# Optimization experiments

Hardware: AMD Instinct MI355X
Metric: run time of the kernel (lower is better)

The kernel has to match this reference:

```python
import jax, jax.numpy as jnp
import numpy as np

B, O, D = 4096, 256, 256  # batch, size_out (rules), size_in (features)


def setup_inputs() -> dict:
    key = jax.random.key(0)
    k1, k2, k3, k4, k5 = jax.random.split(key, 5)
    return {
        "x": jax.random.normal(k1, (B, D), dtype=jnp.float32),
        "scales": jax.random.normal(k2, (O, D), dtype=jnp.float32),
        # strict upper triangle holds the packed rot vectors (original inits them to zeros;
        # small values keep the quadratic form well conditioned)
        "rots": jax.random.normal(k3, (O, D, D), dtype=jnp.float32) * 0.02,
        "centroids": jax.random.normal(k4, (O, D, 1), dtype=jnp.float32),
        "b": jax.random.uniform(k5, (O,), dtype=jnp.float32, minval=0.5, maxval=1.5),
    }


def reference(x, scales, rots, centroids, b):
    # Build symmetric transform A[o] = diag(scales[o]) + triu(rots[o],1) + triu(rots[o],1)^T
    # (equivalent to the loop of diag_embed(r_i, i+1) + mirrored lower diagonal).
    upper = jnp.triu(rots, 1)                                   # [O,D,D]
    A = upper + jnp.swapaxes(upper, -1, -2)
    A = A + jnp.eye(D, dtype=scales.dtype) * scales[:, None, :]  # diag_embed(scales)
    # Augmented affine map: mul[o,i,b'] = A[o] @ x[b'] + centroid[o,i]; const row dropped
    # since only the first size_in rows feed the norm.
    y = jnp.einsum('bj,oij->boi', x, A) + centroids[..., 0][None, :, :]  # [B,O,D]
    rx = jnp.sqrt(jnp.sum(y * y, axis=-1))                      # L2 norm over D -> [B,O]
    return 1.0 / (1.0 + rx ** (2.0 * b))                        # bell membership [B,O]
```

## Files before the change

kernel.cpp:

```cpp
#include <hip/hip_runtime.h>
#include <cstdint>
#include <cmath>

#define Bn 4096
#define Dn 256
#define On 256

typedef __bf16 v8bf __attribute__((ext_vector_type(8)));
typedef float  v16f __attribute__((ext_vector_type(16)));
typedef unsigned short us8 __attribute__((ext_vector_type(8)));

__device__ __forceinline__ unsigned short f2bf(float f) {
    unsigned int u = __builtin_bit_cast(unsigned int, f);
    unsigned int r = (u + 0x7fffu + ((u >> 16) & 1u)) >> 16;
    return (unsigned short)r;
}

__device__ __forceinline__ void gl_lds16(const void* g, void* l) {
    __builtin_amdgcn_global_load_lds(
        (const __attribute__((address_space(1))) void*)(uintptr_t)g,
        (__attribute__((address_space(3))) void*)(uintptr_t)l, 16, 0, 0);
}

__global__ __launch_bounds__(256) void prep_x(const float* __restrict__ x,
                                              unsigned short* __restrict__ xbT) {
    __shared__ float t[64][68];
    const int tid = threadIdx.x;
    const int bb = blockIdx.x >> 2;
    const int kb = blockIdx.x & 3;
    const int b0 = bb * 64;
#pragma unroll
    for (int s = 0; s < 4; ++s) {
        const int idx = s * 256 + tid;
        const int r = idx >> 4, c4 = idx & 15;
        const float4 v = *(const float4*)(x + (size_t)(b0 + r) * Dn + kb * 64 + c4 * 4);
        *(float4*)&t[r][c4 * 4] = v;
    }
    __syncthreads();
    const int lane = tid & 63, wv = tid >> 6;
#pragma unroll
    for (int s = 0; s < 2; ++s) {
        const int kcl = s * 4 + wv;
        us8 u;
#pragma unroll
        for (int q = 0; q < 8; ++q) u[q] = f2bf(t[lane][kcl * 8 + q]);
        *(us8*)(xbT + ((size_t)(kb * 8 + kcl) * Bn + b0 + lane) * 8) = u;
    }
}

template <int TI, int TJ>
__device__ __forceinline__ void extract_pair(const float* T, v8bf (&af)[16],
                                             float sc, int wv, int lane) {
    const int l31 = lane & 31, hw = lane >> 5;
    const int half = wv & 1, grp = wv >> 1;
    if (TI == TJ) {
        if (grp == TI) {
            const int r = half * 32 + l31;
            const int mr = (r & 7) << 2;
#pragma unroll
            for (int kq = 0; kq < 4; ++kq) {
                us8 u;
#pragma unroll
                for (int q = 0; q < 8; ++q) {
                    const int c = kq * 16 + hw * 8 + q;
                    const float v = (r < c) ? T[r * 64 + (c ^ mr)]
                                  : ((r > c) ? T[c * 64 + (r ^ ((c & 7) << 2))]
                                             : sc);
                    u[q] = f2bf(v);
                }
                af[TI * 4 + kq] = __builtin_bit_cast(v8bf, u);
            }
        }
    } else {
        if (grp == TI) {
            const int r = half * 32 + l31;
            const int mr = (r & 7) << 2;
#pragma unroll
            for (int kq = 0; kq < 4; ++kq) {
                const int c0 = kq * 16 + hw * 8;
                const float4 a = *(const float4*)&T[r * 64 + (c0 ^ mr)];
                const float4 b = *(const float4*)&T[r * 64 + ((c0 + 4) ^ mr)];
                us8 u;
                u[0] = f2bf(a.x); u[1] = f2bf(a.y); u[2] = f2bf(a.z); u[3] = f2bf(a.w);
                u[4] = f2bf(b.x); u[5] = f2bf(b.y); u[6] = f2bf(b.z); u[7] = f2bf(b.w);
                af[TJ * 4 + kq] = __builtin_bit_cast(v8bf, u);
            }
        } else if (grp == TJ) {
            const int cL = half * 32 + l31;
#pragma unroll
            for (int kq = 0; kq < 4; ++kq) {
                us8 u;
#pragma unroll
                for (int q = 0; q < 8; ++q) {
                    const int rL = kq * 16 + hw * 8 + q;
                    u[q] = f2bf(T[rL * 64 + (cL ^ ((rL & 7) << 2))]);
                }
                af[TI * 4 + kq] = __builtin_bit_cast(v8bf, u);
            }
        }
    }
}

#define WAITV(N)                                              \
    do {                                                      \
        asm volatile("s_waitcnt vmcnt(" #N ")" ::: "memory"); \
        __builtin_amdgcn_sched_barrier(0);                    \
    } while (0)
#define LGKM0()                                               \
    do {                                                      \
        asm volatile("s_waitcnt lgkmcnt(0)" ::: "memory");    \
        __builtin_amdgcn_sched_barrier(0);                    \
    } while (0)
#define BARF()                                                \
    do {                                                      \
        __builtin_amdgcn_sched_barrier(0);                    \
        __builtin_amdgcn_s_barrier();                         \
        __builtin_amdgcn_sched_barrier(0);                    \
    } while (0)

#define STAGE_T(TIv, TJv, DST)                                               \
    do {                                                                     \
        const float* s_ = rbase + (TIv) * (64 * Dn) + (TJv) * 64;            \
        _Pragma("unroll")                                                    \
        for (int s = 0; s < 2; ++s) {                                        \
            const int idx = s * 512 + tid;                                   \
            const int r = idx >> 4, c4 = idx & 15;                           \
            gl_lds16(s_ + (size_t)r * Dn + ((c4 ^ (r & 7)) * 4),             \
                     (DST) + idx * 4);                                       \
        }                                                                    \
    } while (0)

__global__ __launch_bounds__(512, 4) void fuzzy_main(
    const float* __restrict__ rots, const float* __restrict__ scales,
    const unsigned short* __restrict__ xbT, const float* __restrict__ cent,
    const float* __restrict__ bvals, float* __restrict__ out) {
    __shared__ __align__(16) unsigned short Xs[2][2048][8];
    __shared__ float ssbuf[2][8][64];
    __shared__ float centL[Dn];

    const int tid  = threadIdx.x;
    const int lane = tid & 63;
    const int wv   = tid >> 6;
    const int l31  = lane & 31, hw = lane >> 5;
    const int Lb = blockIdx.x;
    const int o     = (Lb & 7) * 32 + ((Lb >> 3) & 31);
    const int bhalf = Lb >> 8;
    const int bh0   = bhalf * 2048;

    if (tid < Dn) centL[tid] = cent[o * Dn + tid];
    const float sc = scales[o * Dn + wv * 32 + l31];
    const float bv = bvals[o];

    WAITV(0);

    float* const S0 = (float*)&Xs[0][0][0];
    float* const S1 = S0 + 4096;
    float* const S2 = (float*)&Xs[1][0][0];
    float* const S3 = S2 + 4096;
    const float* const rbase = rots + ((size_t)o << 16);

    v8bf af[16];

    STAGE_T(0, 1, S0); STAGE_T(2, 3, S1);
    STAGE_T(0, 2, S2); STAGE_T(1, 3, S3);
    WAITV(4); BARF();
    extract_pair<0, 1>(S0, af, sc, wv, lane);
    extract_pair<2, 3>(S1, af, sc, wv, lane);
    LGKM0(); BARF();
    STAGE_T(0, 3, S0); STAGE_T(1, 2, S1);
    WAITV(4); BARF();
    extract_pair<0, 2>(S2, af, sc, wv, lane);
    extract_pair<1, 3>(S3, af, sc, wv, lane);
    LGKM0(); BARF();
    STAGE_T(0, 0, S2); STAGE_T(1, 1, S3);
    WAITV(4); BARF();
    extract_pair<0, 3>(S0, af, sc, wv, lane);
    extract_pair<1, 2>(S1, af, sc, wv, lane);
    LGKM0(); BARF();
    STAGE_T(2, 2, S0); STAGE_T(3, 3, S1);
    WAITV(4); BARF();
    extract_pair<0, 0>(S2, af, sc, wv, lane);
    extract_pair<1, 1>(S3, af, sc, wv, lane);
    LGKM0(); BARF();
    WAITV(0); BARF();
    extract_pair<2, 2>(S0, af, sc, wv, lane);
    extract_pair<3, 3>(S1, af, sc, wv, lane);
    LGKM0(); BARF();

    const unsigned short* px[4];
#pragma unroll
    for (int s = 0; s < 4; ++s)
        px[s] = xbT + ((size_t)(s * 8 + wv) * Bn + bh0 + lane) * 8;

#pragma unroll
    for (int s = 0; s < 4; ++s)
        gl_lds16(px[s], &Xs[0][s * 512 + tid][0]);
    __syncthreads();

    for (int it = 0; it < 32; ++it) {
        const int buf = it & 1;
        if (it < 31) {
#pragma unroll
            for (int s = 0; s < 4; ++s) {
                px[s] += 512;
                gl_lds16(px[s], &Xs[buf ^ 1][s * 512 + tid][0]);
            }
        }

        if (it >= 1 && lane < 8) {
            const int bl = wv * 8 + lane;
            float ssq = 0.f;
#pragma unroll
            for (int w = 0; w < 8; ++w) ssq += ssbuf[buf ^ 1][w][bl];
            out[(size_t)(bh0 + (it - 1) * 64 + bl) * On + o] =
                1.0f / (1.0f + exp2f(bv * log2f(ssq)));
        }

        v16f acc[2];
#pragma unroll
        for (int nt = 0; nt < 2; ++nt)
#pragma unroll
            for (int rg = 0; rg < 16; ++rg) acc[nt][rg] = 0.f;

#pragma unroll
        for (int ks = 0; ks < 16; ++ks) {
            const v8bf xf0 = *(const v8bf*)&Xs[buf][(ks * 2 + hw) * 64 + l31][0];
            const v8bf xf1 = *(const v8bf*)&Xs[buf][(ks * 2 + hw) * 64 + 32 + l31][0];
            acc[0] = __builtin_amdgcn_mfma_f32_32x32x16_bf16(af[ks], xf0, acc[0], 0, 0, 0);
            acc[1] = __builtin_amdgcn_mfma_f32_32x32x16_bf16(af[ks], xf1, acc[1], 0, 0, 0);
        }

#pragma unroll
        for (int nt = 0; nt < 2; ++nt) {
            float v = 0.f;
#pragma unroll
            for (int g = 0; g < 4; ++g) {
                const float4 c4 = *(const float4*)&centL[wv * 32 + 8 * g + 4 * hw];
                float y;
                y = acc[nt][g * 4 + 0] + c4.x; v = fmaf(y, y, v);
                y = acc[nt][g * 4 + 1] + c4.y; v = fmaf(y, y, v);
                y = acc[nt][g * 4 + 2] + c4.z; v = fmaf(y, y, v);
                y = acc[nt][g * 4 + 3] + c4.w; v = fmaf(y, y, v);
            }
            v += __shfl_xor(v, 32);
            if (lane < 32) ssbuf[buf][wv][nt * 32 + lane] = v;
        }
        __syncthreads();
    }
    if (lane < 8) {
        const int bl = wv * 8 + lane;
        float ssq = 0.f;
#pragma unroll
        for (int w = 0; w < 8; ++w) ssq += ssbuf[1][w][bl];
        out[(size_t)(bh0 + 31 * 64 + bl) * On + o] =
            1.0f / (1.0f + exp2f(bv * log2f(ssq)));
    }
}

__global__ void fallback_kernel(const float* __restrict__ x, const float* __restrict__ scales,
                                const float* __restrict__ rots, const float* __restrict__ cent,
                                const float* __restrict__ bvals, float* __restrict__ out) {
    const int b = blockIdx.x * blockDim.x + threadIdx.x;
    const int o = blockIdx.y;
    if (b >= Bn) return;
    const float* R  = rots + (size_t)o * Dn * Dn;
    const float* xv = x + (size_t)b * Dn;
    float ss = 0.f;
    for (int i = 0; i < Dn; ++i) {
        float a = cent[o * Dn + i];
        for (int j = 0; j < Dn; ++j) {
            const float w = (j > i) ? R[i * Dn + j]
                          : ((j < i) ? R[j * Dn + i] : scales[o * Dn + i]);
            a += w * xv[j];
        }
        ss += a * a;
    }
    out[(size_t)b * On + o] = 1.f / (1.f + powf(ss, bvals[o]));
}

extern "C" void kernel_launch(void* const* d_in, const int* in_sizes, int n_in,
                              void* d_out, int out_size, void* d_ws, size_t ws_size,
                              hipStream_t stream) {
    const float* x         = (const float*)d_in[0];
    const float* scales    = (const float*)d_in[1];
    const float* rots      = (const float*)d_in[2];
    const float* centroids = (const float*)d_in[3];
    const float* bvals     = (const float*)d_in[4];
    float* out = (float*)d_out;

    const size_t needX = (size_t)Bn * Dn * sizeof(unsigned short);

    if (ws_size >= needX) {
        unsigned short* xbT = (unsigned short*)d_ws;
        prep_x<<<dim3(256), 256, 0, stream>>>(x, xbT);
        fuzzy_main<<<dim3(512), 512, 0, stream>>>(rots, scales, xbT, centroids, bvals, out);
    } else {
        fallback_kernel<<<dim3(Bn / 256, On), 256, 0, stream>>>(x, scales, rots, centroids,
                                                                bvals, out);
    }
}
```

Measured before the change: 236.2 us.

## Deepen X staging to four 32-column buffers with split accumulators

The batch loop now moves in 32-column steps through a four-deep LDS ring of X tiles, with three tiles in flight, in place of a double buffer of 64-column tiles. Each step runs one MFMA chain split across two alternating accumulators to shorten dependency chains, and it raises wave priority around the MFMA loop. Barriers now sit behind counted vmcnt waits, so global loads overlap the compute of earlier tiles. The cost is twice as many loop iterations and barriers, fewer MFMAs per iteration, and smaller but more frequent output stores.

```diff
diff --git a/kernel.cpp b/kernel.cpp
--- a/kernel.cpp
+++ b/kernel.cpp
@@ -130,12 +130,21 @@
         }                                                                    \
     } while (0)
 
+#define STAGE_X(BUF)                                                         \
+    do {                                                                     \
+        _Pragma("unroll")                                                    \
+        for (int s = 0; s < 2; ++s) {                                        \
+            gl_lds16(px[s], &Xs[BUF][s * 512 + tid][0]);                     \
+            px[s] += 256;                  \
+        }                                                                    \
+    } while (0)
+
 __global__ __launch_bounds__(512, 4) void fuzzy_main(
     const float* __restrict__ rots, const float* __restrict__ scales,
     const unsigned short* __restrict__ xbT, const float* __restrict__ cent,
     const float* __restrict__ bvals, float* __restrict__ out) {
-    __shared__ __align__(16) unsigned short Xs[2][2048][8];
-    __shared__ float ssbuf[2][8][64];
+    __shared__ __align__(16) unsigned short Xs[4][1024][8];
+    __shared__ float ssbuf[2][8][32];
     __shared__ float centL[Dn];
 
     const int tid  = threadIdx.x;
@@ -154,9 +163,9 @@
     WAITV(0);
 
     float* const S0 = (float*)&Xs[0][0][0];
-    float* const S1 = S0 + 4096;
-    float* const S2 = (float*)&Xs[1][0][0];
-    float* const S3 = S2 + 4096;
+    float* const S1 = (float*)&Xs[1][0][0];
+    float* const S2 = (float*)&Xs[2][0][0];
+    float* const S3 = (float*)&Xs[3][0][0];
     const float* const rbase = rots + ((size_t)o << 16);
 
     v8bf af[16];
@@ -187,72 +196,71 @@
     extract_pair<3, 3>(S1, af, sc, wv, lane);
     LGKM0(); BARF();
 
-    const unsigned short* px[4];
-#pragma unroll
-    for (int s = 0; s < 4; ++s)
-        px[s] = xbT + ((size_t)(s * 8 + wv) * Bn + bh0 + lane) * 8;
-
-#pragma unroll
-    for (int s = 0; s < 4; ++s)
-        gl_lds16(px[s], &Xs[0][s * 512 + tid][0]);
-    __syncthreads();
-
-    for (int it = 0; it < 32; ++it) {
-        const int buf = it & 1;
-        if (it < 31) {
-#pragma unroll
-            for (int s = 0; s < 4; ++s) {
-                px[s] += 512;
-                gl_lds16(px[s], &Xs[buf ^ 1][s * 512 + tid][0]);
-            }
-        }
-
-        if (it >= 1 && lane < 8) {
-            const int bl = wv * 8 + lane;
+    const unsigned short* px[2];
+#pragma unroll
+    for (int s = 0; s < 2; ++s) {
+        const int idx = s * 512 + tid;
+        px[s] = xbT + ((size_t)(idx >> 5) * Bn + bh0 + (idx & 31)) * 8;
+    }
+
+    STAGE_X(0); STAGE_X(1); STAGE_X(2);
+    WAITV(4);
+    LGKM0(); BARF();
+
+    for (int t = 0; t < 64; ++t) {
+        const int buf = t & 3;
+        if (t <= 60) STAGE_X((t + 3) & 3);
+
+        if (t >= 1 && lane < 4) {
+            const int bl = wv * 4 + lane;
             float ssq = 0.f;
 #pragma unroll
-            for (int w = 0; w < 8; ++w) ssq += ssbuf[buf ^ 1][w][bl];
-            out[(size_t)(bh0 + (it - 1) * 64 + bl) * On + o] =
+            for (int w = 0; w < 8; ++w) ssq += ssbuf[(t - 1) & 1][w][bl];
+            out[(size_t)(bh0 + (t - 1) * 32 + bl) * On + o] =
                 1.0f / (1.0f + exp2f(bv * log2f(ssq)));
         }
 
-        v16f acc[2];
-#pragma unroll
-        for (int nt = 0; nt < 2; ++nt)
-#pragma unroll
-            for (int rg = 0; rg < 16; ++rg) acc[nt][rg] = 0.f;
-
+        v16f a0, a1;
+#pragma unroll
+        for (int rg = 0; rg < 16; ++rg) { a0[rg] = 0.f; a1[rg] = 0.f; }
+        __builtin_amdgcn_s_setprio(1);
 #pragma unroll
         for (int ks = 0; ks < 16; ++ks) {
-            const v8bf xf0 = *(const v8bf*)&Xs[buf][(ks * 2 + hw) * 64 + l31][0];
-            const v8bf xf1 = *(const v8bf*)&Xs[buf][(ks * 2 + hw) * 64 + 32 + l31][0];
-            acc[0] = __builtin_amdgcn_mfma_f32_32x32x16_bf16(af[ks], xf0, acc[0], 0, 0, 0);
-            acc[1] = __builtin_amdgcn_mfma_f32_32x32x16_bf16(af[ks], xf1, acc[1], 0, 0, 0);
-        }
-
-#pragma unroll
-        for (int nt = 0; nt < 2; ++nt) {
+            const v8bf xf = *(const v8bf*)&Xs[buf][(ks * 2 + hw) * 32 + l31][0];
+            if (ks & 1)
+                a1 = __builtin_amdgcn_mfma_f32_32x32x16_bf16(af[ks], xf, a1, 0, 0, 0);
+            else
+                a0 = __builtin_amdgcn_mfma_f32_32x32x16_bf16(af[ks], xf, a0, 0, 0, 0);
+        }
+        __builtin_amdgcn_s_setprio(0);
+
+        {
             float v = 0.f;
 #pragma unroll
             for (int g = 0; g < 4; ++g) {
                 const float4 c4 = *(const float4*)&centL[wv * 32 + 8 * g + 4 * hw];
                 float y;
-                y = acc[nt][g * 4 + 0] + c4.x; v = fmaf(y, y, v);
-                y = acc[nt][g * 4 + 1] + c4.y; v = fmaf(y, y, v);
-                y = acc[nt][g * 4 + 2] + c4.z; v = fmaf(y, y, v);
-                y = acc[nt][g * 4 + 3] + c4.w; v = fmaf(y, y, v);
+                y = a0[g * 4 + 0] + a1[g * 4 + 0] + c4.x; v = fmaf(y, y, v);
+                y = a0[g * 4 + 1] + a1[g * 4 + 1] + c4.y; v = fmaf(y, y, v);
+                y = a0[g * 4 + 2] + a1[g * 4 + 2] + c4.z; v = fmaf(y, y, v);
+                y = a0[g * 4 + 3] + a1[g * 4 + 3] + c4.w; v = fmaf(y, y, v);
             }
             v += __shfl_xor(v, 32);
-            if (lane < 32) ssbuf[buf][wv][nt * 32 + lane] = v;
-        }
-        __syncthreads();
-    }
-    if (lane < 8) {
-        const int bl = wv * 8 + lane;
+            if (lane < 32) ssbuf[t & 1][wv][l31] = v;
+        }
+
+        if (t < 61)      WAITV(4);
+        else if (t == 61) WAITV(2);
+        else              WAITV(0);
+        LGKM0(); BARF();
+    }
+
+    if (lane < 4) {
+        const int bl = wv * 4 + lane;
         float ssq = 0.f;
 #pragma unroll
         for (int w = 0; w < 8; ++w) ssq += ssbuf[1][w][bl];
-        out[(size_t)(bh0 + 31 * 64 + bl) * On + o] =
+        out[(size_t)(bh0 + 63 * 32 + bl) * On + o] =
             1.0f / (1.0f + exp2f(bv * log2f(ssq)));
     }
 }
```

Result: no change. 232.3 us (-1.7%).
